# Kernel optimization log

Hardware: AMD Instinct MI355X
Metric: run time of the kernel (lower is better)

Reference implementation:

```python
import jax, jax.numpy as jnp
import numpy as np

V = 128   # vocab / number of symbols (len(index_map))
N = 512   # number of automaton states
L = 4096  # input string length


def setup_inputs() -> dict:
    key = jax.random.key(0)
    k0, k1, k2, k3, k4 = jax.random.split(key, 5)
    tokens = jax.random.randint(k0, (L,), 0, V, dtype=jnp.int32)
    # start distribution over states
    start = jax.nn.softmax(jax.random.normal(k1, (N,), dtype=jnp.float32))
    # row-stochastic transition matrices, one per symbol: [V, N, N]
    transfer = jax.nn.softmax(jax.random.normal(k2, (V, N, N), dtype=jnp.float32), axis=-1)
    # per-symbol prob vectors near 1.0 so the running product stays finite: [V, N]
    probs = 0.9 + 0.2 * jax.random.uniform(k3, (V, N), dtype=jnp.float32)
    # final acceptance vector: [N]
    finals = jax.random.uniform(k4, (N,), dtype=jnp.float32)
    return {"tokens": tokens, "start": start, "transfer": transfer,
            "probs": probs, "finals": finals}


def reference(tokens, start, transfer, probs, finals):
    # Faithful device-side version of the Python loop:
    #   prob *= internal @ prob_tensors[sym]; internal = internal @ transfer_tensors[sym]
    # index_map is identity (symbol == tensor index). Whole walk is one lax.scan,
    # removing the per-step host sync of the original.
    def step(carry, t):
        internal, prob = carry
        prob = prob * jnp.dot(internal, probs[t])          # scalar emission prob
        internal = jnp.dot(internal, transfer[t])          # [N] @ [N,N] -> [N]
        return (internal, prob), None

    init = (start, jnp.float32(1.0))
    (internal, prob), _ = jax.lax.scan(step, init, tokens)
    prob = prob * jnp.dot(internal, finals)
    return internal, prob
```

## Files before the change

### kernel.cpp

```cpp
#include <hip/hip_runtime.h>
#include <stdint.h>


typedef unsigned short ushort_t;
typedef __attribute__((ext_vector_type(8))) short v8s;
typedef __attribute__((ext_vector_type(4))) float f32x4;

#define NSTATE 512
#define NSYM   128
#define LTOK   4096
#define MS     ((size_t)NSTATE*NSTATE)

__device__ __forceinline__ ushort_t f2bf(float f){
  unsigned u = __float_as_uint(f);
  u = u + 0x7FFFu + ((u >> 16) & 1u);
  return (ushort_t)(u >> 16);
}
__device__ __forceinline__ float bf2f(ushort_t h){
  return __uint_as_float(((unsigned)h) << 16);
}
__device__ __forceinline__ size_t fragT_idx(int m, int k){
  return ((size_t)((k >> 5)*512 + m)*4 + ((k >> 3) & 3))*8 + (k & 7);
}

__device__ __forceinline__ void step_mfma(f32x4 acc[4][8],
    const ushort_t* __restrict__ As, const ushort_t* __restrict__ Bf,
    int wv, int l15, int q4){
  const ushort_t* base = Bf + ((size_t)(wv*64 + l15)*4 + q4)*8;
  v8s aA[4], aN[4];
  #pragma unroll
  for (int mt = 0; mt < 4; ++mt) aA[mt] = *(const v8s*)&base[mt*512];
  #pragma unroll
  for (int kk = 0; kk < 16; ++kk){
    if (kk < 15){
      #pragma unroll
      for (int mt = 0; mt < 4; ++mt)
        aN[mt] = *(const v8s*)&base[(size_t)(kk+1)*16384 + mt*512];
    }
    #pragma unroll
    for (int nt = 0; nt < 8; ++nt){
      int n  = nt*16 + l15;
      int ch = kk*4 + q4;
      v8s bf = *(const v8s*)&As[n*512 + ((ch ^ (n & 7))*8)];
      #pragma unroll
      for (int mt = 0; mt < 4; ++mt)
        acc[mt][nt] = __builtin_amdgcn_mfma_f32_16x16x32_bf16(aA[mt], bf, acc[mt][nt], 0,0,0);
    }
    #pragma unroll
    for (int mt = 0; mt < 4; ++mt) aA[mt] = aN[mt];
  }
}

__device__ __forceinline__ void load_strip(ushort_t* As,
    const ushort_t* __restrict__ src, int rowbase, int tid){
  #pragma unroll
  for (int q = 0; q < 16; ++q){
    int F = tid + q*512;
    int m = F >> 6, p = F & 63;
    *(v8s*)&As[m*512 + p*8] =
      *(const v8s*)&src[(size_t)(rowbase + m)*NSTATE + ((p ^ (m & 7))*8)];
  }
}

__device__ __forceinline__ void writeback_lds(ushort_t* As, f32x4 acc[4][8],
    int wv, int l15, int q4){
  #pragma unroll
  for (int nt = 0; nt < 8; ++nt){
    int n = nt*16 + l15;
    #pragma unroll
    for (int mt = 0; mt < 4; ++mt){
      int col = wv*64 + mt*16 + q4*4;
      ushort4 h;
      h.x = f2bf(acc[mt][nt][0]); h.y = f2bf(acc[mt][nt][1]);
      h.z = f2bf(acc[mt][nt][2]); h.w = f2bf(acc[mt][nt][3]);
      int p = (col >> 3) ^ (n & 7);
      *(ushort4*)&As[n*512 + p*8 + (col & 7)] = h;
    }
  }
}

__device__ __forceinline__ void store_out(ushort_t* slot, f32x4 acc[4][8],
    int rowbase, bool even, int lane, int wv, int l15, int q4){
  if (even){
    #pragma unroll
    for (int nt = 0; nt < 8; ++nt){
      int grow = rowbase + nt*16 + l15;
      #pragma unroll
      for (int mt = 0; mt < 4; ++mt){
        int gcol = wv*64 + mt*16 + q4*4;
        ushort4 h;
        h.x = f2bf(acc[mt][nt][0]); h.y = f2bf(acc[mt][nt][1]);
        h.z = f2bf(acc[mt][nt][2]); h.w = f2bf(acc[mt][nt][3]);
        *(ushort4*)&slot[(size_t)grow*NSTATE + gcol] = h;
      }
    }
  } else {
    #pragma unroll
    for (int nt = 0; nt < 8; ++nt){
      int G0 = rowbase + nt*16 + (l15 & 12);
      #pragma unroll
      for (int mt = 0; mt < 4; ++mt){
        float v0 = acc[mt][nt][0], v1 = acc[mt][nt][1];
        float v2 = acc[mt][nt][2], v3 = acc[mt][nt][3];
        float s0 = __shfl_xor(v0, 2), s1 = __shfl_xor(v1, 2);
        float s2 = __shfl_xor(v2, 2), s3 = __shfl_xor(v3, 2);
        const bool h2 = lane & 2;
        float c0 = h2 ? s2 : v0, c1 = h2 ? s3 : v1;
        float c2 = h2 ? v2 : s0, c3 = h2 ? v3 : s1;
        float u0 = __shfl_xor(c0, 1), u1 = __shfl_xor(c1, 1);
        float u2 = __shfl_xor(c2, 1), u3 = __shfl_xor(c3, 1);
        const bool h1 = lane & 1;
        float d0 = h1 ? u1 : c0, d1 = h1 ? c1 : u0;
        float d2 = h1 ? u3 : c2, d3 = h1 ? c3 : u2;
        int mcol = wv*64 + mt*16 + q4*4 + (lane & 3);
        ushort4 h;
        h.x = f2bf(d0); h.y = f2bf(d1); h.z = f2bf(d2); h.w = f2bf(d3);
        *(ushort4*)&slot[fragT_idx(mcol, G0)] = h;
      }
    }
  }
}

__global__ __launch_bounds__(512, 2) void k_chain2(
    const int* __restrict__ tokens, const ushort_t* __restrict__ Tb,
    const ushort_t* __restrict__ Tf, ushort_t* __restrict__ Lout, int W){
  extern __shared__ __align__(16) ushort_t As[];
  const int b = blockIdx.x;
  const int c       = (b >> 5) * 8 + (b & 7);
  const int rowbase = ((b >> 3) & 3) * 128;
  const int tid  = threadIdx.x;
  const int lane = tid & 63;
  const int wv   = tid >> 6;
  const int l15  = lane & 15;
  const int q4   = lane >> 4;
  const int t0   = c * W;

  load_strip(As, Tb + (size_t)tokens[t0] * MS, rowbase, tid);
  __syncthreads();
  for (int k = 1; k < W; ++k){
    f32x4 acc[4][8];
    #pragma unroll
    for (int mt = 0; mt < 4; ++mt)
      #pragma unroll
      for (int nt = 0; nt < 8; ++nt) acc[mt][nt] = (f32x4){0.f,0.f,0.f,0.f};
    step_mfma(acc, As, Tf + (size_t)tokens[t0 + k] * MS, wv, l15, q4);
    __syncthreads();
    if (k < W - 1){
      writeback_lds(As, acc, wv, l15, q4);
      __syncthreads();
    } else {
      store_out(Lout + (size_t)c * MS, acc, rowbase, !(c & 1), lane, wv, l15, q4);
    }
  }
}

__global__ __launch_bounds__(512, 2) void k_tree2(
    const ushort_t* __restrict__ Lsrc, ushort_t* __restrict__ Ldst){
  extern __shared__ __align__(16) ushort_t As[];
  const int j = blockIdx.x >> 2, rowbase = (blockIdx.x & 3) * 128;
  const int tid  = threadIdx.x;
  const int lane = tid & 63;
  const int wv   = tid >> 6;
  const int l15  = lane & 15;
  const int q4   = lane >> 4;
  load_strip(As, Lsrc + (size_t)(2*j) * MS, rowbase, tid);
  __syncthreads();
  f32x4 acc[4][8];
  #pragma unroll
  for (int mt = 0; mt < 4; ++mt)
    #pragma unroll
    for (int nt = 0; nt < 8; ++nt) acc[mt][nt] = (f32x4){0.f,0.f,0.f,0.f};
  step_mfma(acc, As, Lsrc + (size_t)(2*j + 1) * MS, wv, l15, q4);
  store_out(Ldst + (size_t)j * MS, acc, rowbase, !(j & 1), lane, wv, l15, q4);
}

__global__ __launch_bounds__(256) void k_prep(const float* __restrict__ transfer,
                                              ushort_t* __restrict__ Tb,
                                              ushort_t* __restrict__ Tf){
  __shared__ ushort_t t[32*512];
  const int s = blockIdx.x >> 4;
  const int kk = blockIdx.x & 15;
  const int krows = kk * 32;
  const int tid = threadIdx.x;
  for (int idx = tid; idx < 32*512; idx += 256){
    int r = idx >> 9, n = idx & 511;
    ushort_t h = f2bf(transfer[(size_t)s*MS + (size_t)(krows + r)*NSTATE + n]);
    Tb[(size_t)s*MS + (size_t)(krows + r)*NSTATE + n] = h;
    t[r*512 + n] = h;
  }
  __syncthreads();
  for (int idx = tid; idx < 512*4; idx += 256){
    int n = idx >> 2, cc = idx & 3;
    v8s vv;
    #pragma unroll
    for (int jj = 0; jj < 8; ++jj) vv[jj] = (short)t[(cc*8 + jj)*512 + n];
    *(v8s*)&Tf[(size_t)s*MS + ((size_t)(kk*512 + n)*4 + cc)*8] = vv;
  }
}

__device__ __forceinline__ void gl_lds16(const void* g, void* l){
  __builtin_amdgcn_global_load_lds(
      (const __attribute__((address_space(1))) unsigned int*)g,
      (__attribute__((address_space(3))) unsigned int*)l, 16, 0, 0);
}

__device__ void gemm_step(const ushort_t* __restrict__ A,
                          const ushort_t* __restrict__ Bf,
                          ushort_t* dRM, ushort_t* dT, int rowbase){
  __shared__ __align__(16) ushort_t ldsA[128*64];
  __shared__ __align__(16) ushort_t ldsB[128*64];
  const int tid  = threadIdx.x;
  const int lane = tid & 63;
  const int w    = tid >> 6;
  const int l15  = lane & 15;
  const int koff = (lane >> 4) * 8;

  __threadfence_block();

  for (int p = 0; p < 4; ++p){
    f32x4 acc[2][8];
    #pragma unroll
    for (int rt = 0; rt < 2; ++rt)
      #pragma unroll
      for (int ct = 0; ct < 8; ++ct) acc[rt][ct] = (f32x4){0.f,0.f,0.f,0.f};

    for (int kk = 0; kk < 8; ++kk){
      __syncthreads();
      #pragma unroll
      for (int q = 0; q < 4; ++q){
        int idx = tid + q*256;
        int rr = idx >> 3, cch = idx & 7;
        gl_lds16(&A [(size_t)(rowbase + rr)*NSTATE + kk*64 + cch*8], &ldsA[idx*8]);
        gl_lds16(&Bf[fragT_idx(p*128 + rr, kk*64 + cch*8)], &ldsB[idx*8]);
      }
      __syncthreads();
      #pragma unroll
      for (int kc = 0; kc < 2; ++kc){
        v8s a0 = *(const v8s*)&ldsA[(w*32 +      l15)*64 + kc*32 + koff];
        v8s a1 = *(const v8s*)&ldsA[(w*32 + 16 + l15)*64 + kc*32 + koff];
        #pragma unroll
        for (int ct = 0; ct < 8; ++ct){
          v8s bb = *(const v8s*)&ldsB[(ct*16 + l15)*64 + kc*32 + koff];
          acc[0][ct] = __builtin_amdgcn_mfma_f32_16x16x32_bf16(a0, bb, acc[0][ct], 0,0,0);
          acc[1][ct] = __builtin_amdgcn_mfma_f32_16x16x32_bf16(a1, bb, acc[1][ct], 0,0,0);
        }
      }
    }
    const int rb = rowbase + w*32 + (lane >> 4)*4;
    #pragma unroll
    for (int rt = 0; rt < 2; ++rt)
      #pragma unroll
      for (int ct = 0; ct < 8; ++ct)
        #pragma unroll
        for (int i = 0; i < 4; ++i){
          int grow = rb + rt*16 + i;
          int gcol = p*128 + ct*16 + l15;
          ushort_t h = f2bf(acc[rt][ct][i]);
          if (dRM) dRM[(size_t)grow*NSTATE + gcol] = h;
          if (dT)  dT [fragT_idx(gcol, grow)] = h;
        }
  }
  __syncthreads();
}

__global__ __launch_bounds__(256) void k_chain(const int* __restrict__ tokens,
    const ushort_t* __restrict__ Tb, const ushort_t* __restrict__ Tf,
    ushort_t* ping, ushort_t* pong, ushort_t* Lout, int W){
  const int c = blockIdx.x >> 2;
  const int r = blockIdx.x & 3;
  const int t0 = c * W;
  ushort_t* bufA = ping + (size_t)c * MS;
  ushort_t* bufB = pong + (size_t)c * MS;
  for (int k = 1; k < W; ++k){
    const ushort_t* Asrc = (k == 1) ? Tb + (size_t)tokens[t0] * MS
                                    : (((k - 1) & 1) ? bufA : bufB);
    ushort_t *dRM, *dT;
    if (k == W - 1){
      ushort_t* slot = Lout + (size_t)c * MS;
      dRM = (c & 1) ? nullptr : slot;
      dT  = (c & 1) ? slot    : nullptr;
    } else {
      dRM = (k & 1) ? bufA : bufB; dT = nullptr;
    }
    gemm_step(Asrc, Tf + (size_t)tokens[t0 + k] * MS, dRM, dT, r * 128);
  }
}

__global__ __launch_bounds__(256) void k_tree(const ushort_t* __restrict__ Lsrc,
                                              ushort_t* __restrict__ Ldst){
  const int j = blockIdx.x >> 2, r = blockIdx.x & 3;
  const ushort_t* A  = Lsrc + (size_t)(2*j)     * MS;
  const ushort_t* Bf = Lsrc + (size_t)(2*j + 1) * MS;
  ushort_t* slot = Ldst + (size_t)j * MS;
  gemm_step(A, Bf, (j & 1) ? nullptr : slot, (j & 1) ? slot : nullptr, r * 128);
}

__global__ __launch_bounds__(512) void k_descent(const float* __restrict__ start,
    const ushort_t* __restrict__ lvl4, const ushort_t* __restrict__ Upper,
    float* __restrict__ u, int baseLvl){
  __shared__ float v[NSTATE];
  const int upOff[7] = {0,128,192,224,240,248,252};
  const int g = blockIdx.x, tid = threadIdx.x;
  v[tid] = start[tid];
  __syncthreads();
  int pos = 0;
  for (int p = 11 - baseLvl; p >= 0; --p){
    if ((g >> p) & 1){
      const int L = baseLvl + p;
      const ushort_t* arr = (L == 4) ? lvl4 : (Upper + (size_t)upOff[L-5] * MS);
      const ushort_t* M = arr + (size_t)(pos >> p) * MS;
      float a0=0.f,a1=0.f,a2=0.f,a3=0.f;
      #pragma unroll 4
      for (int i = 0; i < NSTATE; i += 4){
        a0 += v[i  ] * bf2f(M[(size_t)(i  )*NSTATE + tid]);
        a1 += v[i+1] * bf2f(M[(size_t)(i+1)*NSTATE + tid]);
        a2 += v[i+2] * bf2f(M[(size_t)(i+2)*NSTATE + tid]);
        a3 += v[i+3] * bf2f(M[(size_t)(i+3)*NSTATE + tid]);
      }
      __syncthreads();
      v[tid] = (a0+a1)+(a2+a3);
      __syncthreads();
      pos += 1 << p;
    }
  }
  u[(size_t)g*NSTATE + tid] = v[tid];
}

__global__ __launch_bounds__(512) void k_phase2(const int* __restrict__ tokens,
    const float* __restrict__ u, const ushort_t* __restrict__ Tb,
    const float* __restrict__ probs, float* __restrict__ partials,
    float* __restrict__ out, int SEG){
  __shared__ float v[NSTATE];
  __shared__ float redc[8], redm[8];
  __shared__ float fac, minv;
  const int g = blockIdx.x, tid = threadIdx.x;
  v[tid] = u[(size_t)g*NSTATE + tid];
  float pp = 1.f;
  __syncthreads();
  for (int k = 0; k < SEG; ++k){
    const int tok = tokens[g*SEG + k];
    float a = v[tid];
    float bb = a * probs[(size_t)tok*NSTATE + tid];
    #pragma unroll
    for (int o = 32; o > 0; o >>= 1){
      a  += __shfl_down(a, o);
      bb += __shfl_down(bb, o);
    }
    if ((tid & 63) == 0){ redm[tid >> 6] = a; redc[tid >> 6] = bb; }
    __syncthreads();
    if (tid == 0){
      float m = 0.f, cc = 0.f;
      #pragma unroll
      for (int q = 0; q < 8; ++q){ m += redm[q]; cc += redc[q]; }
      fac = cc / m;
    }
    __syncthreads();
    pp *= fac;
    const ushort_t* M = Tb + (size_t)tok * MS;
    float a0=0.f,a1=0.f,a2=0.f,a3=0.f;
    #pragma unroll 4
    for (int i = 0; i < NSTATE; i += 4){
      a0 += v[i  ] * bf2f(M[(size_t)(i  )*NSTATE + tid]);
      a1 += v[i+1] * bf2f(M[(size_t)(i+1)*NSTATE + tid]);
      a2 += v[i+2] * bf2f(M[(size_t)(i+2)*NSTATE + tid]);
      a3 += v[i+3] * bf2f(M[(size_t)(i+3)*NSTATE + tid]);
    }
    __syncthreads();
    v[tid] = (a0+a1)+(a2+a3);
    __syncthreads();
  }
  if (tid == 0) partials[g] = pp;
  if (g == gridDim.x - 1){
    float a = v[tid];
    #pragma unroll
    for (int o = 32; o > 0; o >>= 1) a += __shfl_down(a, o);
    if ((tid & 63) == 0) redm[tid >> 6] = a;
    __syncthreads();
    if (tid == 0){
      float m = 0.f;
      #pragma unroll
      for (int q = 0; q < 8; ++q) m += redm[q];
      minv = 1.f / m;
    }
    __syncthreads();
    out[tid] = v[tid] * minv;
  }
}

__global__ __launch_bounds__(512) void k_finish(const float* __restrict__ partials,
    const float* __restrict__ finals, float* out, int G){
  __shared__ float red[8];
  const int tid = threadIdx.x;
  float x = out[tid] * finals[tid];
  #pragma unroll
  for (int o = 32; o > 0; o >>= 1) x += __shfl_down(x, o);
  if ((tid & 63) == 0) red[tid >> 6] = x;
  __syncthreads();
  if (tid == 0){
    float s = 0.f;
    for (int q = 0; q < 8; ++q) s += red[q];
    float pp = 1.f;
    for (int q = 0; q < G; ++q) pp *= partials[q];
    out[NSTATE] = pp * s;
  }
}

__global__ __launch_bounds__(512) void k_fallback(const int* __restrict__ tokens,
    const float* __restrict__ start, const float* __restrict__ transfer,
    const float* __restrict__ probs, const float* __restrict__ finals,
    float* out){
  __shared__ float v[NSTATE];
  __shared__ float red[9];
  const int tid = threadIdx.x;
  v[tid] = start[tid];
  float pp = 1.f;
  __syncthreads();
  for (int t = 0; t < LTOK; ++t){
    const int tok = tokens[t];
    float x = v[tid] * probs[(size_t)tok*NSTATE + tid];
    #pragma unroll
    for (int o = 32; o > 0; o >>= 1) x += __shfl_down(x, o);
    if ((tid & 63) == 0) red[tid >> 6] = x;
    __syncthreads();
    if (tid == 0){
      float cc = 0.f;
      for (int q = 0; q < 8; ++q) cc += red[q];
      red[8] = cc;
    }
    __syncthreads();
    pp *= red[8];
    const float* M = transfer + (size_t)tok * MS;
    float acc = 0.f;
    #pragma unroll 8
    for (int i = 0; i < NSTATE; ++i) acc += v[i] * M[(size_t)i*NSTATE + tid];
    __syncthreads();
    v[tid] = acc;
    __syncthreads();
  }
  out[tid] = v[tid];
  float x = v[tid] * finals[tid];
  #pragma unroll
  for (int o = 32; o > 0; o >>= 1) x += __shfl_down(x, o);
  if ((tid & 63) == 0) red[tid >> 6] = x;
  __syncthreads();
  if (tid == 0){
    float s = 0.f;
    for (int q = 0; q < 8; ++q) s += red[q];
    out[NSTATE] = pp * s;
  }
}

extern "C" void kernel_launch(void* const* d_in, const int* in_sizes, int n_in,
                              void* d_out, int out_size, void* d_ws, size_t ws_size,
                              hipStream_t stream) {
  const int*   tokens   = (const int*)  d_in[0];
  const float* start    = (const float*)d_in[1];
  const float* transfer = (const float*)d_in[2];
  const float* probs    = (const float*)d_in[3];
  const float* finals   = (const float*)d_in[4];
  float* out = (float*)d_out;
  (void)in_sizes; (void)n_in; (void)out_size;

  const size_t C2 = MS * 2;
  size_t off = 0;
  const size_t o_Tb    = off; off += C2 * NSYM;
  const size_t o_Tf    = off; off += C2 * NSYM;
  const size_t o_Upper = off; off += C2 * 254;
  const size_t o_u     = off; off += (size_t)256 * NSTATE * 4;
  const size_t o_part  = off; off += 256 * 4 + 256;
  const size_t common  = off;

  const int LDSBYTES = 128*512*2;
  bool bigLds =
    hipFuncSetAttribute(reinterpret_cast<const void*>(k_chain2),
        hipFuncAttributeMaxDynamicSharedMemorySize, LDSBYTES) == hipSuccess &&
    hipFuncSetAttribute(reinterpret_cast<const void*>(k_tree2),
        hipFuncAttributeMaxDynamicSharedMemorySize, LDSBYTES) == hipSuccess;

  char* ws = (char*)d_ws;
  ushort_t* Tb    = (ushort_t*)(ws + o_Tb);
  ushort_t* Tf    = (ushort_t*)(ws + o_Tf);
  ushort_t* Upper = (ushort_t*)(ws + o_Upper);
  float*    u     = (float*)   (ws + o_u);
  float*    parts = (float*)   (ws + o_part);

  const int upOff[7] = {0,128,192,224,240,248,252};
  ushort_t* lvl[12] = {nullptr};
  for (int l = 5; l <= 11; ++l) lvl[l] = Upper + (size_t)upOff[l-5] * MS;

  int W = 0, sLvl = 0;
  size_t oo = common;
  if (bigLds){
    if      (ws_size >= common + C2 * (512 + 256)) { W = 8;  sLvl = 3; }
    else if (ws_size >= common + C2 * 256)         { W = 16; sLvl = 4; }
    else if (ws_size >= common)                    { W = 32; sLvl = 5; }
    if (W){
      if (W == 8) { lvl[3] = (ushort_t*)(ws + oo); oo += C2 * 512; }
      if (W <= 16){ lvl[4] = (ushort_t*)(ws + oo); oo += C2 * 256; }
    }
  } else {
    if (ws_size >= common + C2 * 256) { W = 32; sLvl = 5; }
  }
  if (!W){
    k_fallback<<<1, 512, 0, stream>>>(tokens, start, transfer, probs, finals, out);
    return;
  }
  const int nchain = LTOK / W;
  const int G    = lvl[4] ? 256 : 128;
  const int SEGc = LTOK / G;
  const int baseLvl = lvl[4] ? 4 : 5;

  k_prep<<<NSYM * 16, 256, 0, stream>>>(transfer, Tb, Tf);
  if (bigLds){
    k_chain2<<<nchain * 4, 512, LDSBYTES, stream>>>(tokens, Tb, Tf, lvl[sLvl], W);
    for (int l = sLvl; l < 11; ++l){
      const int cntNext = LTOK >> (l + 1);
      k_tree2<<<cntNext * 4, 512, LDSBYTES, stream>>>(lvl[l], lvl[l + 1]);
    }
  } else {
    ushort_t* ping = (ushort_t*)(ws + oo); oo += C2 * nchain;
    ushort_t* pong = (ushort_t*)(ws + oo); oo += C2 * nchain;
    k_chain<<<nchain * 4, 256, 0, stream>>>(tokens, Tb, Tf, ping, pong, lvl[sLvl], W);
    for (int l = sLvl; l < 11; ++l){
      const int cntNext = LTOK >> (l + 1);
      k_tree<<<cntNext * 4, 256, 0, stream>>>(lvl[l], lvl[l + 1]);
    }
  }
  k_descent<<<G, 512, 0, stream>>>(start, lvl[4], Upper, u, baseLvl);
  k_phase2 <<<G, 512, 0, stream>>>(tokens, u, Tb, probs, parts, out, SEGc);
  k_finish <<<1, 512, 0, stream>>>(parts, finals, out, G);
}
```

Measured before the change: 1.867 ms.

## Halve row strips in chain/tree kernels and vectorize phase2 matvec reads

The chain and tree matrix-product kernels now give each block a 64-row strip instead of 128. LDS drops to 64 KB and launch bounds allow 4 blocks per CU, with twice as many blocks launched. The aim is more occupancy and parallelism, at the cost of reloading the right-hand matrix twice as often per output. Separately, k_phase2 now reads the fragment-transposed Tf layout with 16-byte vector loads instead of strided scalar bf16 loads from Tb.

```diff
diff --git a/kernel.cpp b/kernel.cpp
--- a/kernel.cpp
+++ b/kernel.cpp
@@ -23,7 +23,7 @@
   return ((size_t)((k >> 5)*512 + m)*4 + ((k >> 3) & 3))*8 + (k & 7);
 }
 
-__device__ __forceinline__ void step_mfma(f32x4 acc[4][8],
+__device__ __forceinline__ void step_mfma64(f32x4 acc[4][4],
     const ushort_t* __restrict__ As, const ushort_t* __restrict__ Bf,
     int wv, int l15, int q4){
   const ushort_t* base = Bf + ((size_t)(wv*64 + l15)*4 + q4)*8;
@@ -38,7 +38,7 @@
         aN[mt] = *(const v8s*)&base[(size_t)(kk+1)*16384 + mt*512];
     }
     #pragma unroll
-    for (int nt = 0; nt < 8; ++nt){
+    for (int nt = 0; nt < 4; ++nt){
       int n  = nt*16 + l15;
       int ch = kk*4 + q4;
       v8s bf = *(const v8s*)&As[n*512 + ((ch ^ (n & 7))*8)];
@@ -51,10 +51,10 @@
   }
 }
 
-__device__ __forceinline__ void load_strip(ushort_t* As,
+__device__ __forceinline__ void load_strip64(ushort_t* As,
     const ushort_t* __restrict__ src, int rowbase, int tid){
   #pragma unroll
-  for (int q = 0; q < 16; ++q){
+  for (int q = 0; q < 8; ++q){
     int F = tid + q*512;
     int m = F >> 6, p = F & 63;
     *(v8s*)&As[m*512 + p*8] =
@@ -62,10 +62,10 @@
   }
 }
 
-__device__ __forceinline__ void writeback_lds(ushort_t* As, f32x4 acc[4][8],
+__device__ __forceinline__ void writeback64(ushort_t* As, f32x4 acc[4][4],
     int wv, int l15, int q4){
   #pragma unroll
-  for (int nt = 0; nt < 8; ++nt){
+  for (int nt = 0; nt < 4; ++nt){
     int n = nt*16 + l15;
     #pragma unroll
     for (int mt = 0; mt < 4; ++mt){
@@ -79,11 +79,11 @@
   }
 }
 
-__device__ __forceinline__ void store_out(ushort_t* slot, f32x4 acc[4][8],
+__device__ __forceinline__ void store_out64(ushort_t* slot, f32x4 acc[4][4],
     int rowbase, bool even, int lane, int wv, int l15, int q4){
   if (even){
     #pragma unroll
-    for (int nt = 0; nt < 8; ++nt){
+    for (int nt = 0; nt < 4; ++nt){
       int grow = rowbase + nt*16 + l15;
       #pragma unroll
       for (int mt = 0; mt < 4; ++mt){
@@ -96,7 +96,7 @@
     }
   } else {
     #pragma unroll
-    for (int nt = 0; nt < 8; ++nt){
+    for (int nt = 0; nt < 4; ++nt){
       int G0 = rowbase + nt*16 + (l15 & 12);
       #pragma unroll
       for (int mt = 0; mt < 4; ++mt){
@@ -121,13 +121,13 @@
   }
 }
 
-__global__ __launch_bounds__(512, 2) void k_chain2(
+__global__ __launch_bounds__(512, 4) void k_chain3(
     const int* __restrict__ tokens, const ushort_t* __restrict__ Tb,
     const ushort_t* __restrict__ Tf, ushort_t* __restrict__ Lout, int W){
   extern __shared__ __align__(16) ushort_t As[];
   const int b = blockIdx.x;
-  const int c       = (b >> 5) * 8 + (b & 7);
-  const int rowbase = ((b >> 3) & 3) * 128;
+  const int c       = (b >> 6) * 8 + (b & 7);
+  const int rowbase = ((b >> 3) & 7) * 64;
   const int tid  = threadIdx.x;
   const int lane = tid & 63;
   const int wv   = tid >> 6;
@@ -135,43 +135,47 @@
   const int q4   = lane >> 4;
   const int t0   = c * W;
 
-  load_strip(As, Tb + (size_t)tokens[t0] * MS, rowbase, tid);
+  load_strip64(As, Tb + (size_t)tokens[t0] * MS, rowbase, tid);
   __syncthreads();
   for (int k = 1; k < W; ++k){
-    f32x4 acc[4][8];
+    f32x4 acc[4][4];
     #pragma unroll
     for (int mt = 0; mt < 4; ++mt)
       #pragma unroll
-      for (int nt = 0; nt < 8; ++nt) acc[mt][nt] = (f32x4){0.f,0.f,0.f,0.f};
-    step_mfma(acc, As, Tf + (size_t)tokens[t0 + k] * MS, wv, l15, q4);
+      for (int nt = 0; nt < 4; ++nt) acc[mt][nt] = (f32x4){0.f,0.f,0.f,0.f};
+    step_mfma64(acc, As, Tf + (size_t)tokens[t0 + k] * MS, wv, l15, q4);
     __syncthreads();
     if (k < W - 1){
-      writeback_lds(As, acc, wv, l15, q4);
+      writeback64(As, acc, wv, l15, q4);
       __syncthreads();
     } else {
-      store_out(Lout + (size_t)c * MS, acc, rowbase, !(c & 1), lane, wv, l15, q4);
-    }
-  }
-}
-
-__global__ __launch_bounds__(512, 2) void k_tree2(
+      store_out64(Lout + (size_t)c * MS, acc, rowbase, !(c & 1), lane, wv, l15, q4);
+    }
+  }
+}
+
+__global__ __launch_bounds__(512, 4) void k_tree3(
     const ushort_t* __restrict__ Lsrc, ushort_t* __restrict__ Ldst){
   extern __shared__ __align__(16) ushort_t As[];
-  const int j = blockIdx.x >> 2, rowbase = (blockIdx.x & 3) * 128;
+  const int b = blockIdx.x;
+  int j, strip;
+  if (gridDim.x >= 64){ j = (b >> 6) * 8 + (b & 7); strip = (b >> 3) & 7; }
+  else                { j = b >> 3;                  strip = b & 7; }
+  const int rowbase = strip * 64;
   const int tid  = threadIdx.x;
   const int lane = tid & 63;
   const int wv   = tid >> 6;
   const int l15  = lane & 15;
   const int q4   = lane >> 4;
-  load_strip(As, Lsrc + (size_t)(2*j) * MS, rowbase, tid);
-  __syncthreads();
-  f32x4 acc[4][8];
+  load_strip64(As, Lsrc + (size_t)(2*j) * MS, rowbase, tid);
+  __syncthreads();
+  f32x4 acc[4][4];
   #pragma unroll
   for (int mt = 0; mt < 4; ++mt)
     #pragma unroll
-    for (int nt = 0; nt < 8; ++nt) acc[mt][nt] = (f32x4){0.f,0.f,0.f,0.f};
-  step_mfma(acc, As, Lsrc + (size_t)(2*j + 1) * MS, wv, l15, q4);
-  store_out(Ldst + (size_t)j * MS, acc, rowbase, !(j & 1), lane, wv, l15, q4);
+    for (int nt = 0; nt < 4; ++nt) acc[mt][nt] = (f32x4){0.f,0.f,0.f,0.f};
+  step_mfma64(acc, As, Lsrc + (size_t)(2*j + 1) * MS, wv, l15, q4);
+  store_out64(Ldst + (size_t)j * MS, acc, rowbase, !(j & 1), lane, wv, l15, q4);
 }
 
 __global__ __launch_bounds__(256) void k_prep(const float* __restrict__ transfer,
@@ -327,7 +331,7 @@
 }
 
 __global__ __launch_bounds__(512) void k_phase2(const int* __restrict__ tokens,
-    const float* __restrict__ u, const ushort_t* __restrict__ Tb,
+    const float* __restrict__ u, const ushort_t* __restrict__ Tf,
     const float* __restrict__ probs, float* __restrict__ partials,
     float* __restrict__ out, int SEG){
   __shared__ float v[NSTATE];
@@ -356,14 +360,19 @@
     }
     __syncthreads();
     pp *= fac;
-    const ushort_t* M = Tb + (size_t)tok * MS;
+    const ushort_t* Mf = Tf + (size_t)tok * MS + (size_t)tid * 32;
     float a0=0.f,a1=0.f,a2=0.f,a3=0.f;
-    #pragma unroll 4
-    for (int i = 0; i < NSTATE; i += 4){
-      a0 += v[i  ] * bf2f(M[(size_t)(i  )*NSTATE + tid]);
-      a1 += v[i+1] * bf2f(M[(size_t)(i+1)*NSTATE + tid]);
-      a2 += v[i+2] * bf2f(M[(size_t)(i+2)*NSTATE + tid]);
-      a3 += v[i+3] * bf2f(M[(size_t)(i+3)*NSTATE + tid]);
+    for (int bnd = 0; bnd < 16; ++bnd){
+      const v8s* pv = (const v8s*)&Mf[(size_t)bnd*16384];
+      v8s h0 = pv[0], h1 = pv[1], h2 = pv[2], h3 = pv[3];
+      const float* vb = &v[bnd*32];
+      #pragma unroll
+      for (int j = 0; j < 8; ++j){
+        a0 += vb[j     ] * bf2f((ushort_t)h0[j]);
+        a1 += vb[j +  8] * bf2f((ushort_t)h1[j]);
+        a2 += vb[j + 16] * bf2f((ushort_t)h2[j]);
+        a3 += vb[j + 24] * bf2f((ushort_t)h3[j]);
+      }
     }
     __syncthreads();
     v[tid] = (a0+a1)+(a2+a3);
@@ -470,11 +479,11 @@
   const size_t o_part  = off; off += 256 * 4 + 256;
   const size_t common  = off;
 
-  const int LDSBYTES = 128*512*2;
+  const int LDSBYTES = 64*512*2;
   bool bigLds =
-    hipFuncSetAttribute(reinterpret_cast<const void*>(k_chain2),
+    hipFuncSetAttribute(reinterpret_cast<const void*>(k_chain3),
         hipFuncAttributeMaxDynamicSharedMemorySize, LDSBYTES) == hipSuccess &&
-    hipFuncSetAttribute(reinterpret_cast<const void*>(k_tree2),
+    hipFuncSetAttribute(reinterpret_cast<const void*>(k_tree3),
         hipFuncAttributeMaxDynamicSharedMemorySize, LDSBYTES) == hipSuccess;
 
   char* ws = (char*)d_ws;
@@ -512,10 +521,10 @@
 
   k_prep<<<NSYM * 16, 256, 0, stream>>>(transfer, Tb, Tf);
   if (bigLds){
-    k_chain2<<<nchain * 4, 512, LDSBYTES, stream>>>(tokens, Tb, Tf, lvl[sLvl], W);
+    k_chain3<<<nchain * 8, 512, LDSBYTES, stream>>>(tokens, Tb, Tf, lvl[sLvl], W);
     for (int l = sLvl; l < 11; ++l){
       const int cntNext = LTOK >> (l + 1);
-      k_tree2<<<cntNext * 4, 512, LDSBYTES, stream>>>(lvl[l], lvl[l + 1]);
+      k_tree3<<<cntNext * 8, 512, LDSBYTES, stream>>>(lvl[l], lvl[l + 1]);
     }
   } else {
     ushort_t* ping = (ushort_t*)(ws + oo); oo += C2 * nchain;
@@ -527,6 +536,6 @@
     }
   }
   k_descent<<<G, 512, 0, stream>>>(start, lvl[4], Upper, u, baseLvl);
-  k_phase2 <<<G, 512, 0, stream>>>(tokens, u, Tb, probs, parts, out, SEGc);
+  k_phase2 <<<G, 512, 0, stream>>>(tokens, u, Tf, probs, parts, out, SEGc);
   k_finish <<<1, 512, 0, stream>>>(parts, finals, out, G);
 }
```

After: 1.783 ms. -4.5%, faster.
